# Optimization experiments

Measured on AMD Instinct MI355X. Metric: run time of the kernel, lower is better.

The kernel has to match this reference:

```python
import jax, jax.numpy as jnp
import numpy as np

HEAD_DIM = 128

def setup_inputs() -> dict:
    key = jax.random.key(0)
    k1, k2, k3 = jax.random.split(key, 3)
    B, S, H, Hkv, D = 2, 2048, 32, 8, HEAD_DIM
    q = jax.random.normal(k1, (B, S, H, D), dtype=jnp.float32)
    k = jax.random.normal(k2, (B, S, Hkv, D), dtype=jnp.float32)
    v = jax.random.normal(k3, (B, S, Hkv, D), dtype=jnp.float32)
    return {"q": q, "k": k, "v": v}

def reference(q, k, v):
    # Causal GQA attention, same math as SDPA(is_causal=True, scale=head_dim**-0.5)
    # q: [B,S,H,D], k/v: [B,S,Hkv,D]; H = Hkv * G (grouped-query attention)
    B, S, H, D = q.shape
    Hkv = k.shape[2]
    G = H // Hkv
    scale = jnp.asarray(D, q.dtype) ** -0.5
    qg = q.reshape(B, S, Hkv, G, D)
    # scores: [B, Hkv, G, Sq, Sk]
    scores = jnp.einsum('bqhgd,bkhd->bhgqk', qg, k) * scale
    causal = jnp.tril(jnp.ones((S, S), dtype=bool))  # [Sq, Sk]
    scores = jnp.where(causal, scores, jnp.asarray(-jnp.inf, scores.dtype))
    probs = jax.nn.softmax(scores, axis=-1)
    out = jnp.einsum('bhgqk,bkhd->bqhgd', probs, v)
    return out.reshape(B, S, H, D)
```

## Files before the change

kernel.cpp:

```cpp
#include <hip/hip_runtime.h>
#include <hip/hip_bf16.h>

typedef short bf16x8 __attribute__((ext_vector_type(8)));
typedef float f32x4  __attribute__((ext_vector_type(4)));

#define B_    2
#define S_    2048
#define H_    32
#define HKV_  8
#define D_    128
#define QBLK  64
#define QBLK2 128
#define KVB   32
#define SCALE 0.1275431741f

static __device__ inline float exp2_fast(float x) {
    return __builtin_amdgcn_exp2f(x);
}

static __device__ inline unsigned short f2bf(float f) {
    unsigned u = __builtin_bit_cast(unsigned, f);
    u += 0x7fffu + ((u >> 16) & 1u);
    return (unsigned short)(u >> 16);
}
static __device__ inline unsigned pk2(float a, float b) {
    return (unsigned)f2bf(a) | ((unsigned)f2bf(b) << 16);
}
static __device__ inline short cvt_bf(float f) {
    __hip_bfloat16 h = __float2bfloat16(f);
    return __builtin_bit_cast(short, h);
}
static __device__ inline void gload16(const unsigned char* g, unsigned char* l) {
    __builtin_amdgcn_global_load_lds(
        (const __attribute__((address_space(1))) void*)g,
        (__attribute__((address_space(3))) void*)l, 16, 0, 0);
}

__global__ __launch_bounds__(256) void prep_k(const float* __restrict__ Kg,
                                              unsigned char* __restrict__ Kb) {
    const int s   = blockIdx.x * 256 + threadIdx.x;
    const int seg = s & 15;
    const int kv  = (s >> 4) & (S_ - 1);
    const int bhk = s >> 15;
    const int hk  = bhk & (HKV_ - 1);
    const int b   = bhk >> 3;
    const float* src = Kg + ((size_t)(b * S_ + kv) * HKV_ + hk) * D_ + seg * 8;
    float4 x0 = *(const float4*)(src);
    float4 x1 = *(const float4*)(src + 4);
    uint4 u = { pk2(x0.x, x0.y), pk2(x0.z, x0.w), pk2(x1.x, x1.y), pk2(x1.z, x1.w) };
    *(uint4*)(Kb + ((size_t)(b * HKV_ + hk) * S_ + kv) * 256 + ((seg * 16) ^ ((kv & 7) << 4))) = u;
}

__global__ __launch_bounds__(256) void prep_v(const float* __restrict__ Vg,
                                              unsigned short* __restrict__ Vb) {
    const int blk  = blockIdx.x;
    const int half = blk & 1;
    const int tile = (blk >> 1) & 63;
    const int hk   = (blk >> 7) & (HKV_ - 1);
    const int b    = blk >> 10;
    const int t    = threadIdx.x;
    const int kp0  = (t & 3) * 8;
    const int d    = (t >> 2) + half * 64;
    const int kv0  = tile * KVB;
    unsigned short tmp[8];
#pragma unroll
    for (int j = 0; j < 8; ++j) {
        const int kp = kp0 + j;
        const int kv = (((kp >> 2) & 1) << 4) + ((kp >> 3) << 2) + (kp & 3);
        tmp[j] = f2bf(Vg[((size_t)(b * S_ + kv0 + kv) * HKV_ + hk) * D_ + d]);
    }
    unsigned short* dst = Vb + ((size_t)(b * HKV_ + hk) * 64 + tile) * (128 * 32) + d * 32 + kp0;
    *(uint4*)dst = *(uint4*)tmp;
}

__global__ __launch_bounds__(256) void fattn2(
        const float* __restrict__ Qg, const unsigned char* __restrict__ Kb,
        const unsigned char* __restrict__ Vb, float* __restrict__ Og) {
    __shared__ __align__(16) unsigned char lds[2 * 16384];

    const int tid  = threadIdx.x;
    const int lane = tid & 63;
    const int w    = tid >> 6;
    const int m    = lane & 15;
    const int g    = lane >> 4;
    const int lane16 = lane * 16;

    const int SQ  = S_ / QBLK2;
    const int bid = blockIdx.x;
    const int qt  = (SQ - 1) - (bid >> 6);
    const int hb  = bid & 63;
    const int h   = hb & (H_ - 1);
    const int b   = hb >> 5;
    const int hk  = h >> 2;

    const int qB    = qt * QBLK2;
    const int q0w   = qB + w * 32;
    const int qA    = q0w + m;
    const int qgate = q0w + 31;

    const unsigned char* KbH = Kb + (size_t)(b * HKV_ + hk) * S_ * 256;
    const unsigned char* VbH = Vb + (size_t)(b * HKV_ + hk) * 64 * 8192;

    bf16x8 qfA[4], qfB[4];
    {
        const float* qrowA = Qg + (size_t)((b * S_ + qA) * H_ + h) * D_;
        const float* qrowB = qrowA + (size_t)16 * H_ * D_;
#pragma unroll
        for (int db = 0; db < 4; ++db) {
            const float* pA = qrowA + db * 32 + g * 8;
            const float* pB = qrowB + db * 32 + g * 8;
            float4 a0 = *(const float4*)(pA);
            float4 a1 = *(const float4*)(pA + 4);
            float4 b0 = *(const float4*)(pB);
            float4 b1 = *(const float4*)(pB + 4);
            bf16x8 qa, qb;
            qa[0] = cvt_bf(a0.x * SCALE); qa[1] = cvt_bf(a0.y * SCALE);
            qa[2] = cvt_bf(a0.z * SCALE); qa[3] = cvt_bf(a0.w * SCALE);
            qa[4] = cvt_bf(a1.x * SCALE); qa[5] = cvt_bf(a1.y * SCALE);
            qa[6] = cvt_bf(a1.z * SCALE); qa[7] = cvt_bf(a1.w * SCALE);
            qb[0] = cvt_bf(b0.x * SCALE); qb[1] = cvt_bf(b0.y * SCALE);
            qb[2] = cvt_bf(b0.z * SCALE); qb[3] = cvt_bf(b0.w * SCALE);
            qb[4] = cvt_bf(b1.x * SCALE); qb[5] = cvt_bf(b1.y * SCALE);
            qb[6] = cvt_bf(b1.z * SCALE); qb[7] = cvt_bf(b1.w * SCALE);
            qfA[db] = qa; qfB[db] = qb;
        }
    }

    f32x4 oaccA[8], oaccB[8];
#pragma unroll
    for (int i = 0; i < 8; ++i) {
        oaccA[i] = (f32x4){0.f, 0.f, 0.f, 0.f};
        oaccB[i] = (f32x4){0.f, 0.f, 0.f, 0.f};
    }
    float m_run = 4.0f, lsumA = 0.f, lsumB = 0.f;

#define STAGE(kt, cbuf) do {                                                  \
        const unsigned char* KbT = KbH + (size_t)(kt) * (KVB * 256);          \
        const unsigned char* VbT = VbH + (size_t)(kt) * 8192;                 \
        unsigned char* dK = lds + (cbuf) * 16384;                             \
        unsigned char* dV = dK + 8192;                                        \
        gload16(KbT + (w * 2 + 0) * 1024 + lane16, dK + (w * 2 + 0) * 1024);  \
        gload16(KbT + (w * 2 + 1) * 1024 + lane16, dK + (w * 2 + 1) * 1024);  \
        gload16(VbT + (w * 2 + 0) * 1024 + lane16, dV + (w * 2 + 0) * 1024);  \
        gload16(VbT + (w * 2 + 1) * 1024 + lane16, dV + (w * 2 + 1) * 1024);  \
    } while (0)

    const int nt = (qB + QBLK2) / KVB;
    int cur = 0;
    STAGE(0, 0);
    asm volatile("s_waitcnt vmcnt(0)" ::: "memory");
    __builtin_amdgcn_s_barrier();

    for (int t = 0; t < nt; ++t) {
        const int kv0 = t * KVB;
        if (t + 1 < nt) STAGE(t + 1, cur ^ 1);

        if (kv0 <= qgate) {
            const unsigned char* cK = lds + cur * 16384;
            const unsigned char* cV = cK + 8192;

            const f32x4 cinit = (f32x4){-m_run, -m_run, -m_run, -m_run};
            f32x4 stA0 = cinit, stA1 = cinit, stB0 = cinit, stB1 = cinit;
            const int sw = (m & 7) << 4;
            __builtin_amdgcn_s_setprio(1);
#pragma unroll
            for (int db = 0; db < 4; ++db) {
                bf16x8 kf0 = *(const bf16x8*)(cK + (m     ) * 256 + ((db * 64 + g * 16) ^ sw));
                bf16x8 kf1 = *(const bf16x8*)(cK + (m + 16) * 256 + ((db * 64 + g * 16) ^ sw));
                stA0 = __builtin_amdgcn_mfma_f32_16x16x32_bf16(kf0, qfA[db], stA0, 0, 0, 0);
                stA1 = __builtin_amdgcn_mfma_f32_16x16x32_bf16(kf1, qfA[db], stA1, 0, 0, 0);
                stB0 = __builtin_amdgcn_mfma_f32_16x16x32_bf16(kf0, qfB[db], stB0, 0, 0, 0);
                stB1 = __builtin_amdgcn_mfma_f32_16x16x32_bf16(kf1, qfB[db], stB1, 0, 0, 0);
            }
            __builtin_amdgcn_s_setprio(0);

            if (kv0 + (KVB - 1) > q0w) {
                const int qBrow = qA + 16;
#pragma unroll
                for (int jj = 0; jj < 4; ++jj) {
                    const int kva = kv0 + g * 4 + jj;
                    if (kva      > qA)    stA0[jj] = -1e30f;
                    if (kva + 16 > qA)    stA1[jj] = -1e30f;
                    if (kva      > qBrow) stB0[jj] = -1e30f;
                    if (kva + 16 > qBrow) stB1[jj] = -1e30f;
                }
            }

            float pmax = -1e30f;
#pragma unroll
            for (int jj = 0; jj < 4; ++jj)
                pmax = fmaxf(pmax, fmaxf(fmaxf(stA0[jj], stA1[jj]),
                                         fmaxf(stB0[jj], stB1[jj])));
            if (__any(pmax > 12.0f)) {
                float dm = fmaxf(pmax, __shfl_xor(pmax, 16));
                dm = fmaxf(dm, __shfl_xor(dm, 32));
                dm = fmaxf(dm, 0.0f);
                const float corr = exp2_fast(-dm);
                lsumA *= corr; lsumB *= corr;
                float cj[4];
#pragma unroll
                for (int jj = 0; jj < 4; ++jj) cj[jj] = __shfl(corr, g * 4 + jj);
#pragma unroll
                for (int i = 0; i < 8; ++i)
#pragma unroll
                    for (int jj = 0; jj < 4; ++jj) {
                        oaccA[i][jj] *= cj[jj];
                        oaccB[i][jj] *= cj[jj];
                    }
                m_run += dm;
#pragma unroll
                for (int jj = 0; jj < 4; ++jj) {
                    stA0[jj] -= dm; stA1[jj] -= dm;
                    stB0[jj] -= dm; stB1[jj] -= dm;
                }
            }

#pragma unroll
            for (int jj = 0; jj < 4; ++jj) {
                stA0[jj] = exp2_fast(stA0[jj]);
                stA1[jj] = exp2_fast(stA1[jj]);
                stB0[jj] = exp2_fast(stB0[jj]);
                stB1[jj] = exp2_fast(stB1[jj]);
            }
            lsumA += ((stA0[0] + stA0[1]) + (stA0[2] + stA0[3]))
                   + ((stA1[0] + stA1[1]) + (stA1[2] + stA1[3]));
            lsumB += ((stB0[0] + stB0[1]) + (stB0[2] + stB0[3]))
                   + ((stB1[0] + stB1[1]) + (stB1[2] + stB1[3]));

            bf16x8 paA, paB;
#pragma unroll
            for (int jj = 0; jj < 4; ++jj) {
                paA[jj]     = cvt_bf(stA0[jj]);
                paA[4 + jj] = cvt_bf(stA1[jj]);
                paB[jj]     = cvt_bf(stB0[jj]);
                paB[4 + jj] = cvt_bf(stB1[jj]);
            }

            __builtin_amdgcn_s_setprio(1);
#pragma unroll
            for (int db8 = 0; db8 < 8; ++db8) {
                bf16x8 vf = *(const bf16x8*)(cV + (db8 * 16 + m) * 64 + g * 16);
                oaccA[db8] = __builtin_amdgcn_mfma_f32_16x16x32_bf16(paA, vf, oaccA[db8], 0, 0, 0);
                oaccB[db8] = __builtin_amdgcn_mfma_f32_16x16x32_bf16(paB, vf, oaccB[db8], 0, 0, 0);
            }
            __builtin_amdgcn_s_setprio(0);
        }

        asm volatile("s_waitcnt vmcnt(0)" ::: "memory");
        __builtin_amdgcn_s_barrier();
        cur ^= 1;
    }
#undef STAGE

    lsumA += __shfl_xor(lsumA, 16); lsumA += __shfl_xor(lsumA, 32);
    lsumB += __shfl_xor(lsumB, 16); lsumB += __shfl_xor(lsumB, 32);
    const float rA = 1.0f / lsumA, rB = 1.0f / lsumB;
    float rsA[4], rsB[4];
#pragma unroll
    for (int jj = 0; jj < 4; ++jj) {
        rsA[jj] = __shfl(rA, g * 4 + jj);
        rsB[jj] = __shfl(rB, g * 4 + jj);
    }
#pragma unroll
    for (int db8 = 0; db8 < 8; ++db8) {
#pragma unroll
        for (int jj = 0; jj < 4; ++jj) {
            const int qrA = q0w + g * 4 + jj;
            Og[(size_t)((b * S_ + qrA) * H_ + h) * D_ + db8 * 16 + m]
                = oaccA[db8][jj] * rsA[jj];
            Og[(size_t)((b * S_ + qrA + 16) * H_ + h) * D_ + db8 * 16 + m]
                = oaccB[db8][jj] * rsB[jj];
        }
    }
}

__global__ __launch_bounds__(256) void fattn_fallback(
        const float* __restrict__ Qg, const float* __restrict__ Kg,
        const float* __restrict__ Vg, float* __restrict__ Og) {
    __shared__ __align__(16) unsigned char  sK[32 * 256];
    __shared__ __align__(16) unsigned short sV[128 * 40];
    const int tid  = threadIdx.x;
    const int lane = tid & 63;
    const int w    = tid >> 6;
    const int m    = lane & 15;
    const int g    = lane >> 4;
    const int SQ = S_ / QBLK;
    const int bid = blockIdx.x;
    const int qt  = bid % SQ;
    const int h   = (bid / SQ) % H_;
    const int b   = bid / (SQ * H_);
    const int hk  = h >> 2;
    const int qB    = qt * QBLK;
    const int q0w   = qB + w * 16;
    const int q_abs = q0w + m;
    const float SC = 0.08838834764831845f;
    bf16x8 qf[4];
    {
        const float* qrow = Qg + (size_t)((b * S_ + q_abs) * H_ + h) * D_;
#pragma unroll
        for (int db = 0; db < 4; ++db) {
            const float* p = qrow + db * 32 + g * 8;
            float4 a = *(const float4*)(p);
            float4 c = *(const float4*)(p + 4);
            bf16x8 q8;
            q8[0] = (short)f2bf(a.x * SC); q8[1] = (short)f2bf(a.y * SC);
            q8[2] = (short)f2bf(a.z * SC); q8[3] = (short)f2bf(a.w * SC);
            q8[4] = (short)f2bf(c.x * SC); q8[5] = (short)f2bf(c.y * SC);
            q8[6] = (short)f2bf(c.z * SC); q8[7] = (short)f2bf(c.w * SC);
            qf[db] = q8;
        }
    }
    f32x4 oacc[8];
#pragma unroll
    for (int i = 0; i < 8; ++i) oacc[i] = (f32x4){0.f, 0.f, 0.f, 0.f};
    float m_run = -1e30f, lsum = 0.f;
    const int nt = (qB + QBLK) / KVB;
    for (int t = 0; t < nt; ++t) {
        const int kv0 = t * KVB;
        __syncthreads();
        {
            const int r = tid >> 3, seg = tid & 7;
            const float* src = Kg + (size_t)((b * S_ + kv0 + r) * HKV_ + hk) * D_ + seg * 16;
            float4 x0 = *(const float4*)(src + 0);
            float4 x1 = *(const float4*)(src + 4);
            float4 x2 = *(const float4*)(src + 8);
            float4 x3 = *(const float4*)(src + 12);
            uint4 u0 = { pk2(x0.x,x0.y), pk2(x0.z,x0.w), pk2(x1.x,x1.y), pk2(x1.z,x1.w) };
            uint4 u1 = { pk2(x2.x,x2.y), pk2(x2.z,x2.w), pk2(x3.x,x3.y), pk2(x3.z,x3.w) };
            const int colb = seg * 32;
            const int sw   = (r & 7) << 4;
            *(uint4*)(sK + r * 256 + ((colb     ) ^ sw)) = u0;
            *(uint4*)(sK + r * 256 + ((colb + 16) ^ sw)) = u1;
        }
        {
            const int kv = tid & 31, d0 = (tid >> 5) * 16;
            const int kp = (((kv & 15) >> 2) << 3) + ((kv >> 4) << 2) + (kv & 3);
            const float* src = Vg + (size_t)((b * S_ + kv0 + kv) * HKV_ + hk) * D_ + d0;
#pragma unroll
            for (int i = 0; i < 4; ++i) {
                float4 x = *(const float4*)(src + i * 4);
                const int d = d0 + i * 4;
                sV[(d + 0) * 40 + kp] = f2bf(x.x);
                sV[(d + 1) * 40 + kp] = f2bf(x.y);
                sV[(d + 2) * 40 + kp] = f2bf(x.z);
                sV[(d + 3) * 40 + kp] = f2bf(x.w);
            }
        }
        __syncthreads();
        if (kv0 > q0w + 15) continue;
        f32x4 st0 = (f32x4){0.f,0.f,0.f,0.f}, st1 = st0;
#pragma unroll
        for (int db = 0; db < 4; ++db) {
            const int sw = (m & 7) << 4;
            bf16x8 kf0 = *(const bf16x8*)(sK + (m      ) * 256 + ((db * 64 + g * 16) ^ sw));
            bf16x8 kf1 = *(const bf16x8*)(sK + (m + 16 ) * 256 + ((db * 64 + g * 16) ^ sw));
            st0 = __builtin_amdgcn_mfma_f32_16x16x32_bf16(kf0, qf[db], st0, 0, 0, 0);
            st1 = __builtin_amdgcn_mfma_f32_16x16x32_bf16(kf1, qf[db], st1, 0, 0, 0);
        }
        float p[8];
        float tm = -1e30f;
#pragma unroll
        for (int jj = 0; jj < 4; ++jj) {
            int kva = kv0 + g * 4 + jj;
            float s0 = (kva       <= q_abs) ? st0[jj] : -1e30f;
            float s1 = (kva + 16  <= q_abs) ? st1[jj] : -1e30f;
            p[jj]     = s0;
            p[4 + jj] = s1;
            tm = fmaxf(tm, fmaxf(s0, s1));
        }
        tm = fmaxf(tm, __shfl_xor(tm, 16));
        tm = fmaxf(tm, __shfl_xor(tm, 32));
        const float m_new = fmaxf(m_run, tm);
        const float corr  = __expf(m_run - m_new);
        float ls = 0.f;
#pragma unroll
        for (int i = 0; i < 8; ++i) { float e = __expf(p[i] - m_new); p[i] = e; ls += e; }
        ls += __shfl_xor(ls, 16);
        ls += __shfl_xor(ls, 32);
        lsum  = lsum * corr + ls;
        m_run = m_new;
        float cj[4];
#pragma unroll
        for (int jj = 0; jj < 4; ++jj) cj[jj] = __shfl(corr, g * 4 + jj);
#pragma unroll
        for (int i = 0; i < 8; ++i)
#pragma unroll
            for (int jj = 0; jj < 4; ++jj) oacc[i][jj] *= cj[jj];
        bf16x8 pa;
#pragma unroll
        for (int i = 0; i < 8; ++i) pa[i] = (short)f2bf(p[i]);
#pragma unroll
        for (int db8 = 0; db8 < 8; ++db8) {
            bf16x8 vf = *(const bf16x8*)((const unsigned char*)sV +
                          (((db8 * 16 + m) * 40 + g * 8) * 2));
            oacc[db8] = __builtin_amdgcn_mfma_f32_16x16x32_bf16(pa, vf, oacc[db8], 0, 0, 0);
        }
    }
    float rs[4];
    const float rinv = 1.0f / lsum;
#pragma unroll
    for (int jj = 0; jj < 4; ++jj) rs[jj] = __shfl(rinv, g * 4 + jj);
#pragma unroll
    for (int db8 = 0; db8 < 8; ++db8) {
#pragma unroll
        for (int jj = 0; jj < 4; ++jj) {
            const int qr = q0w + g * 4 + jj;
            Og[(size_t)((b * S_ + qr) * H_ + h) * D_ + db8 * 16 + m] = oacc[db8][jj] * rs[jj];
        }
    }
}

extern "C" void kernel_launch(void* const* d_in, const int* in_sizes, int n_in,
                              void* d_out, int out_size, void* d_ws, size_t ws_size,
                              hipStream_t stream) {
    const float* q = (const float*)d_in[0];
    const float* k = (const float*)d_in[1];
    const float* v = (const float*)d_in[2];
    float* o = (float*)d_out;

    const size_t KB_BYTES = (size_t)B_ * HKV_ * S_ * 256;
    const size_t VB_BYTES = (size_t)B_ * HKV_ * 64 * 128 * 32 * 2;

    if (ws_size >= KB_BYTES + VB_BYTES) {
        unsigned char*  Kb = (unsigned char*)d_ws;
        unsigned short* Vb = (unsigned short*)((unsigned char*)d_ws + KB_BYTES);
        prep_k<<<2048, 256, 0, stream>>>(k, Kb);
        prep_v<<<2048, 256, 0, stream>>>(v, Vb);
        const int blocks = B_ * H_ * (S_ / QBLK2);
        fattn2<<<blocks, 256, 0, stream>>>(q, Kb, (const unsigned char*)Vb, o);
    } else {
        const int blocks = B_ * H_ * (S_ / QBLK);
        fattn_fallback<<<blocks, 256, 0, stream>>>(q, k, v, o);
    }
}
```

Baseline: 124.2 us.

## Widen KV tiles to 64 and pair causal query tiles per block

Doubles the KV tile to 64 rows, changes the prepacked V layout to padded 80-element rows, and enlarges the LDS double buffer. Each block now handles two query tiles, a long one and a short one (15-pair and pair), so causal work is balanced and the grid shrinks to 512 blocks. Larger tiles halve the barrier and staging overhead per KV row and give more MFMAs per synchronisation. In exchange LDS use rises to 72KB per block and register pressure grows, which may limit occupancy.

```diff
diff --git a/kernel.cpp b/kernel.cpp
--- a/kernel.cpp
+++ b/kernel.cpp
@@ -11,7 +11,7 @@
 #define D_    128
 #define QBLK  64
 #define QBLK2 128
-#define KVB   32
+#define KVB   64
 #define SCALE 0.1275431741f
 
 static __device__ inline float exp2_fast(float x) {
@@ -53,30 +53,32 @@
 
 __global__ __launch_bounds__(256) void prep_v(const float* __restrict__ Vg,
                                               unsigned short* __restrict__ Vb) {
-    const int blk  = blockIdx.x;
-    const int half = blk & 1;
-    const int tile = (blk >> 1) & 63;
-    const int hk   = (blk >> 7) & (HKV_ - 1);
-    const int b    = blk >> 10;
-    const int t    = threadIdx.x;
-    const int kp0  = (t & 3) * 8;
-    const int d    = (t >> 2) + half * 64;
-    const int kv0  = tile * KVB;
+    const int blk     = blockIdx.x;
+    const int quarter = blk & 3;
+    const int tile    = (blk >> 2) & 31;
+    const int hk      = (blk >> 7) & (HKV_ - 1);
+    const int b       = blk >> 10;
+    const int t       = threadIdx.x;
+    const int kp0     = (t & 7) * 8;
+    const int d       = (t >> 3) + quarter * 32;
+    const int kv0     = tile * KVB;
     unsigned short tmp[8];
 #pragma unroll
     for (int j = 0; j < 8; ++j) {
-        const int kp = kp0 + j;
-        const int kv = (((kp >> 2) & 1) << 4) + ((kp >> 3) << 2) + (kp & 3);
+        const int kp    = kp0 + j;
+        const int chunk = kp >> 5;
+        const int wi    = kp & 31;
+        const int kv    = chunk * 32 + (((wi >> 2) & 1) << 4) + ((wi >> 3) << 2) + (wi & 3);
         tmp[j] = f2bf(Vg[((size_t)(b * S_ + kv0 + kv) * HKV_ + hk) * D_ + d]);
     }
-    unsigned short* dst = Vb + ((size_t)(b * HKV_ + hk) * 64 + tile) * (128 * 32) + d * 32 + kp0;
+    unsigned short* dst = Vb + ((size_t)(b * HKV_ + hk) * 32 + tile) * (128 * 80) + d * 80 + kp0;
     *(uint4*)dst = *(uint4*)tmp;
 }
 
-__global__ __launch_bounds__(256) void fattn2(
+__global__ __launch_bounds__(256, 2) void fattn4(
         const float* __restrict__ Qg, const unsigned char* __restrict__ Kb,
         const unsigned char* __restrict__ Vb, float* __restrict__ Og) {
-    __shared__ __align__(16) unsigned char lds[2 * 16384];
+    __shared__ __align__(16) unsigned char lds[2 * 36864];
 
     const int tid  = threadIdx.x;
     const int lane = tid & 63;
@@ -84,194 +86,212 @@
     const int m    = lane & 15;
     const int g    = lane >> 4;
     const int lane16 = lane * 16;
-
-    const int SQ  = S_ / QBLK2;
-    const int bid = blockIdx.x;
-    const int qt  = (SQ - 1) - (bid >> 6);
-    const int hb  = bid & 63;
-    const int h   = hb & (H_ - 1);
-    const int b   = hb >> 5;
-    const int hk  = h >> 2;
-
-    const int qB    = qt * QBLK2;
-    const int q0w   = qB + w * 32;
-    const int qA    = q0w + m;
-    const int qgate = q0w + 31;
+    const int sw   = (m & 7) << 4;
+
+    const int bid  = blockIdx.x;
+    const int pair = bid >> 6;
+    const int hb   = bid & 63;
+    const int h    = hb & (H_ - 1);
+    const int b    = hb >> 5;
+    const int hk   = h >> 2;
 
     const unsigned char* KbH = Kb + (size_t)(b * HKV_ + hk) * S_ * 256;
-    const unsigned char* VbH = Vb + (size_t)(b * HKV_ + hk) * 64 * 8192;
-
-    bf16x8 qfA[4], qfB[4];
-    {
-        const float* qrowA = Qg + (size_t)((b * S_ + qA) * H_ + h) * D_;
-        const float* qrowB = qrowA + (size_t)16 * H_ * D_;
-#pragma unroll
-        for (int db = 0; db < 4; ++db) {
-            const float* pA = qrowA + db * 32 + g * 8;
-            const float* pB = qrowB + db * 32 + g * 8;
-            float4 a0 = *(const float4*)(pA);
-            float4 a1 = *(const float4*)(pA + 4);
-            float4 b0 = *(const float4*)(pB);
-            float4 b1 = *(const float4*)(pB + 4);
-            bf16x8 qa, qb;
-            qa[0] = cvt_bf(a0.x * SCALE); qa[1] = cvt_bf(a0.y * SCALE);
-            qa[2] = cvt_bf(a0.z * SCALE); qa[3] = cvt_bf(a0.w * SCALE);
-            qa[4] = cvt_bf(a1.x * SCALE); qa[5] = cvt_bf(a1.y * SCALE);
-            qa[6] = cvt_bf(a1.z * SCALE); qa[7] = cvt_bf(a1.w * SCALE);
-            qb[0] = cvt_bf(b0.x * SCALE); qb[1] = cvt_bf(b0.y * SCALE);
-            qb[2] = cvt_bf(b0.z * SCALE); qb[3] = cvt_bf(b0.w * SCALE);
-            qb[4] = cvt_bf(b1.x * SCALE); qb[5] = cvt_bf(b1.y * SCALE);
-            qb[6] = cvt_bf(b1.z * SCALE); qb[7] = cvt_bf(b1.w * SCALE);
-            qfA[db] = qa; qfB[db] = qb;
-        }
-    }
-
-    f32x4 oaccA[8], oaccB[8];
-#pragma unroll
-    for (int i = 0; i < 8; ++i) {
-        oaccA[i] = (f32x4){0.f, 0.f, 0.f, 0.f};
-        oaccB[i] = (f32x4){0.f, 0.f, 0.f, 0.f};
-    }
-    float m_run = 4.0f, lsumA = 0.f, lsumB = 0.f;
+    const unsigned char* VbH = Vb + (size_t)(b * HKV_ + hk) * 32 * 20480;
+    const float* QgH = Qg + (size_t)(b * S_ * H_ + h) * D_;
 
 #define STAGE(kt, cbuf) do {                                                  \
-        const unsigned char* KbT = KbH + (size_t)(kt) * (KVB * 256);          \
-        const unsigned char* VbT = VbH + (size_t)(kt) * 8192;                 \
-        unsigned char* dK = lds + (cbuf) * 16384;                             \
-        unsigned char* dV = dK + 8192;                                        \
-        gload16(KbT + (w * 2 + 0) * 1024 + lane16, dK + (w * 2 + 0) * 1024);  \
-        gload16(KbT + (w * 2 + 1) * 1024 + lane16, dK + (w * 2 + 1) * 1024);  \
-        gload16(VbT + (w * 2 + 0) * 1024 + lane16, dV + (w * 2 + 0) * 1024);  \
-        gload16(VbT + (w * 2 + 1) * 1024 + lane16, dV + (w * 2 + 1) * 1024);  \
+        const unsigned char* KbT = KbH + (size_t)(kt) * 16384;                \
+        const unsigned char* VbT = VbH + (size_t)(kt) * 20480;                \
+        unsigned char* dK = lds + (cbuf) * 36864;                             \
+        unsigned char* dV = dK + 16384;                                       \
+        gload16(KbT + (w * 4 + 0) * 1024 + lane16, dK + (w * 4 + 0) * 1024);  \
+        gload16(KbT + (w * 4 + 1) * 1024 + lane16, dK + (w * 4 + 1) * 1024);  \
+        gload16(KbT + (w * 4 + 2) * 1024 + lane16, dK + (w * 4 + 2) * 1024);  \
+        gload16(KbT + (w * 4 + 3) * 1024 + lane16, dK + (w * 4 + 3) * 1024);  \
+        gload16(VbT + (w * 5 + 0) * 1024 + lane16, dV + (w * 5 + 0) * 1024);  \
+        gload16(VbT + (w * 5 + 1) * 1024 + lane16, dV + (w * 5 + 1) * 1024);  \
+        gload16(VbT + (w * 5 + 2) * 1024 + lane16, dV + (w * 5 + 2) * 1024);  \
+        gload16(VbT + (w * 5 + 3) * 1024 + lane16, dV + (w * 5 + 3) * 1024);  \
+        gload16(VbT + (w * 5 + 4) * 1024 + lane16, dV + (w * 5 + 4) * 1024);  \
     } while (0)
 
-    const int nt = (qB + QBLK2) / KVB;
-    int cur = 0;
-    STAGE(0, 0);
-    asm volatile("s_waitcnt vmcnt(0)" ::: "memory");
-    __builtin_amdgcn_s_barrier();
-
-    for (int t = 0; t < nt; ++t) {
-        const int kv0 = t * KVB;
-        if (t + 1 < nt) STAGE(t + 1, cur ^ 1);
-
-        if (kv0 <= qgate) {
-            const unsigned char* cK = lds + cur * 16384;
-            const unsigned char* cV = cK + 8192;
-
-            const f32x4 cinit = (f32x4){-m_run, -m_run, -m_run, -m_run};
-            f32x4 stA0 = cinit, stA1 = cinit, stB0 = cinit, stB1 = cinit;
-            const int sw = (m & 7) << 4;
-            __builtin_amdgcn_s_setprio(1);
+    for (int job = 0; job < 2; ++job) {
+        const int qt    = (job == 0) ? (15 - pair) : pair;
+        const int qB    = qt * QBLK2;
+        const int q0w   = qB + w * 32;
+        const int qA    = q0w + m;
+        const int qgate = q0w + 31;
+
+        bf16x8 qfA[4], qfB[4];
+        {
+            const float* qrowA = QgH + (size_t)qA * H_ * D_;
+            const float* qrowB = qrowA + (size_t)16 * H_ * D_;
 #pragma unroll
             for (int db = 0; db < 4; ++db) {
-                bf16x8 kf0 = *(const bf16x8*)(cK + (m     ) * 256 + ((db * 64 + g * 16) ^ sw));
-                bf16x8 kf1 = *(const bf16x8*)(cK + (m + 16) * 256 + ((db * 64 + g * 16) ^ sw));
-                stA0 = __builtin_amdgcn_mfma_f32_16x16x32_bf16(kf0, qfA[db], stA0, 0, 0, 0);
-                stA1 = __builtin_amdgcn_mfma_f32_16x16x32_bf16(kf1, qfA[db], stA1, 0, 0, 0);
-                stB0 = __builtin_amdgcn_mfma_f32_16x16x32_bf16(kf0, qfB[db], stB0, 0, 0, 0);
-                stB1 = __builtin_amdgcn_mfma_f32_16x16x32_bf16(kf1, qfB[db], stB1, 0, 0, 0);
+                const float* pA = qrowA + db * 32 + g * 8;
+                const float* pB = qrowB + db * 32 + g * 8;
+                float4 a0 = *(const float4*)(pA);
+                float4 a1 = *(const float4*)(pA + 4);
+                float4 b0 = *(const float4*)(pB);
+                float4 b1 = *(const float4*)(pB + 4);
+                bf16x8 qa, qb;
+                qa[0] = cvt_bf(a0.x * SCALE); qa[1] = cvt_bf(a0.y * SCALE);
+                qa[2] = cvt_bf(a0.z * SCALE); qa[3] = cvt_bf(a0.w * SCALE);
+                qa[4] = cvt_bf(a1.x * SCALE); qa[5] = cvt_bf(a1.y * SCALE);
+                qa[6] = cvt_bf(a1.z * SCALE); qa[7] = cvt_bf(a1.w * SCALE);
+                qb[0] = cvt_bf(b0.x * SCALE); qb[1] = cvt_bf(b0.y * SCALE);
+                qb[2] = cvt_bf(b0.z * SCALE); qb[3] = cvt_bf(b0.w * SCALE);
+                qb[4] = cvt_bf(b1.x * SCALE); qb[5] = cvt_bf(b1.y * SCALE);
+                qb[6] = cvt_bf(b1.z * SCALE); qb[7] = cvt_bf(b1.w * SCALE);
+                qfA[db] = qa; qfB[db] = qb;
             }
-            __builtin_amdgcn_s_setprio(0);
-
-            if (kv0 + (KVB - 1) > q0w) {
-                const int qBrow = qA + 16;
-#pragma unroll
-                for (int jj = 0; jj < 4; ++jj) {
-                    const int kva = kv0 + g * 4 + jj;
-                    if (kva      > qA)    stA0[jj] = -1e30f;
-                    if (kva + 16 > qA)    stA1[jj] = -1e30f;
-                    if (kva      > qBrow) stB0[jj] = -1e30f;
-                    if (kva + 16 > qBrow) stB1[jj] = -1e30f;
-                }
-            }
-
-            float pmax = -1e30f;
-#pragma unroll
-            for (int jj = 0; jj < 4; ++jj)
-                pmax = fmaxf(pmax, fmaxf(fmaxf(stA0[jj], stA1[jj]),
-                                         fmaxf(stB0[jj], stB1[jj])));
-            if (__any(pmax > 12.0f)) {
-                float dm = fmaxf(pmax, __shfl_xor(pmax, 16));
-                dm = fmaxf(dm, __shfl_xor(dm, 32));
-                dm = fmaxf(dm, 0.0f);
-                const float corr = exp2_fast(-dm);
-                lsumA *= corr; lsumB *= corr;
-                float cj[4];
-#pragma unroll
-                for (int jj = 0; jj < 4; ++jj) cj[jj] = __shfl(corr, g * 4 + jj);
-#pragma unroll
-                for (int i = 0; i < 8; ++i)
-#pragma unroll
-                    for (int jj = 0; jj < 4; ++jj) {
-                        oaccA[i][jj] *= cj[jj];
-                        oaccB[i][jj] *= cj[jj];
-                    }
-                m_run += dm;
-#pragma unroll
-                for (int jj = 0; jj < 4; ++jj) {
-                    stA0[jj] -= dm; stA1[jj] -= dm;
-                    stB0[jj] -= dm; stB1[jj] -= dm;
-                }
-            }
-
-#pragma unroll
-            for (int jj = 0; jj < 4; ++jj) {
-                stA0[jj] = exp2_fast(stA0[jj]);
-                stA1[jj] = exp2_fast(stA1[jj]);
-                stB0[jj] = exp2_fast(stB0[jj]);
-                stB1[jj] = exp2_fast(stB1[jj]);
-            }
-            lsumA += ((stA0[0] + stA0[1]) + (stA0[2] + stA0[3]))
-                   + ((stA1[0] + stA1[1]) + (stA1[2] + stA1[3]));
-            lsumB += ((stB0[0] + stB0[1]) + (stB0[2] + stB0[3]))
-                   + ((stB1[0] + stB1[1]) + (stB1[2] + stB1[3]));
-
-            bf16x8 paA, paB;
-#pragma unroll
-            for (int jj = 0; jj < 4; ++jj) {
-                paA[jj]     = cvt_bf(stA0[jj]);
-                paA[4 + jj] = cvt_bf(stA1[jj]);
-                paB[jj]     = cvt_bf(stB0[jj]);
-                paB[4 + jj] = cvt_bf(stB1[jj]);
-            }
-
-            __builtin_amdgcn_s_setprio(1);
-#pragma unroll
-            for (int db8 = 0; db8 < 8; ++db8) {
-                bf16x8 vf = *(const bf16x8*)(cV + (db8 * 16 + m) * 64 + g * 16);
-                oaccA[db8] = __builtin_amdgcn_mfma_f32_16x16x32_bf16(paA, vf, oaccA[db8], 0, 0, 0);
-                oaccB[db8] = __builtin_amdgcn_mfma_f32_16x16x32_bf16(paB, vf, oaccB[db8], 0, 0, 0);
-            }
-            __builtin_amdgcn_s_setprio(0);
-        }
-
+        }
+
+        f32x4 oaccA[8], oaccB[8];
+#pragma unroll
+        for (int i = 0; i < 8; ++i) {
+            oaccA[i] = (f32x4){0.f, 0.f, 0.f, 0.f};
+            oaccB[i] = (f32x4){0.f, 0.f, 0.f, 0.f};
+        }
+        float m_run = 4.0f, lsumA = 0.f, lsumB = 0.f;
+
+        const int nt = 2 * (qt + 1);
+        int cur = 0;
+        STAGE(0, 0);
         asm volatile("s_waitcnt vmcnt(0)" ::: "memory");
         __builtin_amdgcn_s_barrier();
-        cur ^= 1;
+
+        for (int t = 0; t < nt; ++t) {
+            const int kv0 = t * KVB;
+            if (t + 1 < nt) STAGE(t + 1, cur ^ 1);
+
+            if (kv0 <= qgate) {
+                const unsigned char* cK = lds + cur * 36864;
+                const unsigned char* cV = cK + 16384;
+
+                const f32x4 cinit = (f32x4){-m_run, -m_run, -m_run, -m_run};
+                f32x4 sA[4], sB[4];
+#pragma unroll
+                for (int s = 0; s < 4; ++s) { sA[s] = cinit; sB[s] = cinit; }
+                __builtin_amdgcn_s_setprio(1);
+#pragma unroll
+                for (int db = 0; db < 4; ++db) {
+                    const int co = (db * 64 + g * 16) ^ sw;
+#pragma unroll
+                    for (int s = 0; s < 4; ++s) {
+                        bf16x8 kf = *(const bf16x8*)(cK + (m + 16 * s) * 256 + co);
+                        sA[s] = __builtin_amdgcn_mfma_f32_16x16x32_bf16(kf, qfA[db], sA[s], 0, 0, 0);
+                        sB[s] = __builtin_amdgcn_mfma_f32_16x16x32_bf16(kf, qfB[db], sB[s], 0, 0, 0);
+                    }
+                }
+                __builtin_amdgcn_s_setprio(0);
+
+                if (kv0 + (KVB - 1) > q0w) {
+                    const int qBrow = qA + 16;
+#pragma unroll
+                    for (int s = 0; s < 4; ++s)
+#pragma unroll
+                        for (int jj = 0; jj < 4; ++jj) {
+                            const int kva = kv0 + 16 * s + g * 4 + jj;
+                            if (kva > qA)    sA[s][jj] = -1e30f;
+                            if (kva > qBrow) sB[s][jj] = -1e30f;
+                        }
+                }
+
+                float pmax = -1e30f;
+#pragma unroll
+                for (int s = 0; s < 4; ++s)
+#pragma unroll
+                    for (int jj = 0; jj < 4; ++jj)
+                        pmax = fmaxf(pmax, fmaxf(sA[s][jj], sB[s][jj]));
+                if (__any(pmax > 12.0f)) {
+                    float dm = fmaxf(pmax, __shfl_xor(pmax, 16));
+                    dm = fmaxf(dm, __shfl_xor(dm, 32));
+                    dm = fmaxf(dm, 0.0f);
+                    const float corr = exp2_fast(-dm);
+                    lsumA *= corr; lsumB *= corr;
+                    float cj[4];
+#pragma unroll
+                    for (int jj = 0; jj < 4; ++jj) cj[jj] = __shfl(corr, g * 4 + jj);
+#pragma unroll
+                    for (int i = 0; i < 8; ++i)
+#pragma unroll
+                        for (int jj = 0; jj < 4; ++jj) {
+                            oaccA[i][jj] *= cj[jj];
+                            oaccB[i][jj] *= cj[jj];
+                        }
+                    m_run += dm;
+#pragma unroll
+                    for (int s = 0; s < 4; ++s)
+#pragma unroll
+                        for (int jj = 0; jj < 4; ++jj) {
+                            sA[s][jj] -= dm; sB[s][jj] -= dm;
+                        }
+                }
+
+#pragma unroll
+                for (int s = 0; s < 4; ++s)
+#pragma unroll
+                    for (int jj = 0; jj < 4; ++jj) {
+                        sA[s][jj] = exp2_fast(sA[s][jj]);
+                        sB[s][jj] = exp2_fast(sB[s][jj]);
+                    }
+#pragma unroll
+                for (int s = 0; s < 4; ++s) {
+                    lsumA += (sA[s][0] + sA[s][1]) + (sA[s][2] + sA[s][3]);
+                    lsumB += (sB[s][0] + sB[s][1]) + (sB[s][2] + sB[s][3]);
+                }
+
+                bf16x8 paA0, paA1, paB0, paB1;
+#pragma unroll
+                for (int jj = 0; jj < 4; ++jj) {
+                    paA0[jj] = cvt_bf(sA[0][jj]); paA0[4 + jj] = cvt_bf(sA[1][jj]);
+                    paA1[jj] = cvt_bf(sA[2][jj]); paA1[4 + jj] = cvt_bf(sA[3][jj]);
+                    paB0[jj] = cvt_bf(sB[0][jj]); paB0[4 + jj] = cvt_bf(sB[1][jj]);
+                    paB1[jj] = cvt_bf(sB[2][jj]); paB1[4 + jj] = cvt_bf(sB[3][jj]);
+                }
+
+                __builtin_amdgcn_s_setprio(1);
+#pragma unroll
+                for (int db8 = 0; db8 < 8; ++db8) {
+                    const unsigned char* vrow = cV + (db8 * 16 + m) * 160 + g * 16;
+                    bf16x8 vf0 = *(const bf16x8*)(vrow);
+                    bf16x8 vf1 = *(const bf16x8*)(vrow + 64);
+                    oaccA[db8] = __builtin_amdgcn_mfma_f32_16x16x32_bf16(paA0, vf0, oaccA[db8], 0, 0, 0);
+                    oaccB[db8] = __builtin_amdgcn_mfma_f32_16x16x32_bf16(paB0, vf0, oaccB[db8], 0, 0, 0);
+                    oaccA[db8] = __builtin_amdgcn_mfma_f32_16x16x32_bf16(paA1, vf1, oaccA[db8], 0, 0, 0);
+                    oaccB[db8] = __builtin_amdgcn_mfma_f32_16x16x32_bf16(paB1, vf1, oaccB[db8], 0, 0, 0);
+                }
+                __builtin_amdgcn_s_setprio(0);
+            }
+
+            asm volatile("s_waitcnt vmcnt(0)" ::: "memory");
+            __builtin_amdgcn_s_barrier();
+            cur ^= 1;
+        }
+
+        lsumA += __shfl_xor(lsumA, 16); lsumA += __shfl_xor(lsumA, 32);
+        lsumB += __shfl_xor(lsumB, 16); lsumB += __shfl_xor(lsumB, 32);
+        const float rA = 1.0f / lsumA, rB = 1.0f / lsumB;
+        float rsA[4], rsB[4];
+#pragma unroll
+        for (int jj = 0; jj < 4; ++jj) {
+            rsA[jj] = __shfl(rA, g * 4 + jj);
+            rsB[jj] = __shfl(rB, g * 4 + jj);
+        }
+#pragma unroll
+        for (int db8 = 0; db8 < 8; ++db8) {
+#pragma unroll
+            for (int jj = 0; jj < 4; ++jj) {
+                const int qrA = q0w + g * 4 + jj;
+                Og[(size_t)((b * S_ + qrA) * H_ + h) * D_ + db8 * 16 + m]
+                    = oaccA[db8][jj] * rsA[jj];
+                Og[(size_t)((b * S_ + qrA + 16) * H_ + h) * D_ + db8 * 16 + m]
+                    = oaccB[db8][jj] * rsB[jj];
+            }
+        }
     }
 #undef STAGE
-
-    lsumA += __shfl_xor(lsumA, 16); lsumA += __shfl_xor(lsumA, 32);
-    lsumB += __shfl_xor(lsumB, 16); lsumB += __shfl_xor(lsumB, 32);
-    const float rA = 1.0f / lsumA, rB = 1.0f / lsumB;
-    float rsA[4], rsB[4];
-#pragma unroll
-    for (int jj = 0; jj < 4; ++jj) {
-        rsA[jj] = __shfl(rA, g * 4 + jj);
-        rsB[jj] = __shfl(rB, g * 4 + jj);
-    }
-#pragma unroll
-    for (int db8 = 0; db8 < 8; ++db8) {
-#pragma unroll
-        for (int jj = 0; jj < 4; ++jj) {
-            const int qrA = q0w + g * 4 + jj;
-            Og[(size_t)((b * S_ + qrA) * H_ + h) * D_ + db8 * 16 + m]
-                = oaccA[db8][jj] * rsA[jj];
-            Og[(size_t)((b * S_ + qrA + 16) * H_ + h) * D_ + db8 * 16 + m]
-                = oaccB[db8][jj] * rsB[jj];
-        }
-    }
 }
 
 __global__ __launch_bounds__(256) void fattn_fallback(
@@ -314,9 +334,9 @@
 #pragma unroll
     for (int i = 0; i < 8; ++i) oacc[i] = (f32x4){0.f, 0.f, 0.f, 0.f};
     float m_run = -1e30f, lsum = 0.f;
-    const int nt = (qB + QBLK) / KVB;
+    const int nt = (qB + QBLK) / 32;
     for (int t = 0; t < nt; ++t) {
-        const int kv0 = t * KVB;
+        const int kv0 = t * 32;
         __syncthreads();
         {
             const int r = tid >> 3, seg = tid & 7;
@@ -328,9 +348,9 @@
             uint4 u0 = { pk2(x0.x,x0.y), pk2(x0.z,x0.w), pk2(x1.x,x1.y), pk2(x1.z,x1.w) };
             uint4 u1 = { pk2(x2.x,x2.y), pk2(x2.z,x2.w), pk2(x3.x,x3.y), pk2(x3.z,x3.w) };
             const int colb = seg * 32;
-            const int sw   = (r & 7) << 4;
-            *(uint4*)(sK + r * 256 + ((colb     ) ^ sw)) = u0;
-            *(uint4*)(sK + r * 256 + ((colb + 16) ^ sw)) = u1;
+            const int swz  = (r & 7) << 4;
+            *(uint4*)(sK + r * 256 + ((colb     ) ^ swz)) = u0;
+            *(uint4*)(sK + r * 256 + ((colb + 16) ^ swz)) = u1;
         }
         {
             const int kv = tid & 31, d0 = (tid >> 5) * 16;
@@ -351,9 +371,9 @@
         f32x4 st0 = (f32x4){0.f,0.f,0.f,0.f}, st1 = st0;
 #pragma unroll
         for (int db = 0; db < 4; ++db) {
-            const int sw = (m & 7) << 4;
-            bf16x8 kf0 = *(const bf16x8*)(sK + (m      ) * 256 + ((db * 64 + g * 16) ^ sw));
-            bf16x8 kf1 = *(const bf16x8*)(sK + (m + 16 ) * 256 + ((db * 64 + g * 16) ^ sw));
+            const int swz = (m & 7) << 4;
+            bf16x8 kf0 = *(const bf16x8*)(sK + (m      ) * 256 + ((db * 64 + g * 16) ^ swz));
+            bf16x8 kf1 = *(const bf16x8*)(sK + (m + 16 ) * 256 + ((db * 64 + g * 16) ^ swz));
             st0 = __builtin_amdgcn_mfma_f32_16x16x32_bf16(kf0, qf[db], st0, 0, 0, 0);
             st1 = __builtin_amdgcn_mfma_f32_16x16x32_bf16(kf1, qf[db], st1, 0, 0, 0);
         }
@@ -419,15 +439,14 @@
     float* o = (float*)d_out;
 
     const size_t KB_BYTES = (size_t)B_ * HKV_ * S_ * 256;
-    const size_t VB_BYTES = (size_t)B_ * HKV_ * 64 * 128 * 32 * 2;
+    const size_t VB_BYTES = (size_t)B_ * HKV_ * 32 * 128 * 80 * 2;
 
     if (ws_size >= KB_BYTES + VB_BYTES) {
         unsigned char*  Kb = (unsigned char*)d_ws;
         unsigned short* Vb = (unsigned short*)((unsigned char*)d_ws + KB_BYTES);
         prep_k<<<2048, 256, 0, stream>>>(k, Kb);
         prep_v<<<2048, 256, 0, stream>>>(v, Vb);
-        const int blocks = B_ * H_ * (S_ / QBLK2);
-        fattn2<<<blocks, 256, 0, stream>>>(q, Kb, (const unsigned char*)Vb, o);
+        fattn4<<<512, 256, 0, stream>>>(q, Kb, (const unsigned char*)Vb, o);
     } else {
         const int blocks = B_ * H_ * (S_ / QBLK);
         fattn_fallback<<<blocks, 256, 0, stream>>>(q, k, v, o);
```

After: 103.7 us, median of 3. 1.2x faster.
